# Optimization experiments

Measured on AMD Instinct MI355X. Metric: run time of the kernel, lower is better.

Reference implementation:

```python
import jax, jax.numpy as jnp
import numpy as np

INTERVAL = 4
Q = 2 ** INTERVAL          # 16, quantization step
L = 2 ** (8 - INTERVAL) + 1  # 17, LUT size per axis


def round_ste(x):
    # round in forward, identity in backward (BPDA)
    return x + jax.lax.stop_gradient(jnp.round(x) - x)


def setup_inputs() -> dict:
    key = jax.random.key(0)
    k1, k2, k3 = jax.random.split(key, 3)
    # pixel values in [0, 255)
    img = jax.random.uniform(k1, (2, 3, 1080, 1920), jnp.float32) * 255.0
    # int8 LUT / 127 -> values in [-1, 1], shape [L^3, 3, 1, 1]
    lut = jax.random.uniform(k2, (L ** 3, 3, 1, 1), jnp.float32, -1.0, 1.0)
    # color correction matrix, scaled so final output mostly lands in [0,1]
    ccm = (jnp.eye(3, dtype=jnp.float32) + 0.05 * jax.random.normal(k3, (3, 3), jnp.float32)) / 127.0
    return {"img": img, "lut": lut, "ccm": ccm}


def _lut3d_interp(img, lut):
    """Trilinear 3D-LUT interpolation (InterpTorch3DBatch). img: [B,3,H,W]."""
    B, C, H, W = img.shape
    # _prepare_3d_lut_weights: scale, round with STE, clamp
    w = jnp.clip(round_ste(lut * 127.0), -127.0, 127.0)[:, :, 0, 0]  # [L^3, 3]
    flat = img.transpose(0, 2, 3, 1).reshape(-1, 3)  # [N, 3] per-pixel rgb
    r, g, b = flat[:, 0], flat[:, 1], flat[:, 2]
    r1 = jnp.floor(r / Q).astype(jnp.int32)
    g1 = jnp.floor(g / Q).astype(jnp.int32)
    b1 = jnp.floor(b / Q).astype(jnp.int32)
    fr = jnp.mod(r, float(Q))
    fg = jnp.mod(g, float(Q))
    fb = jnp.mod(b, float(Q))
    r2 = jnp.clip(r1 + 1, 0, L - 1)
    g2 = jnp.clip(g1 + 1, 0, L - 1)
    b2 = jnp.clip(b1 + 1, 0, L - 1)

    def corner(i, j, k):
        return w[i * (L * L) + j * L + k]  # [N, 3] gather

    p000 = corner(r1, g1, b1); p001 = corner(r1, g1, b2)
    p010 = corner(r1, g2, b1); p011 = corner(r1, g2, b2)
    p100 = corner(r2, g1, b1); p101 = corner(r2, g1, b2)
    p110 = corner(r2, g2, b1); p111 = corner(r2, g2, b2)

    fr = (fr / Q)[:, None]; fg = (fg / Q)[:, None]; fb = (fb / Q)[:, None]
    c00 = p000 * (1 - fr) + p100 * fr
    c01 = p001 * (1 - fr) + p101 * fr
    c10 = p010 * (1 - fr) + p110 * fr
    c11 = p011 * (1 - fr) + p111 * fr
    c0 = c00 * (1 - fg) + c10 * fg
    c1 = c01 * (1 - fg) + c11 * fg
    out = c0 * (1 - fb) + c1 * fb  # [N, 3]
    return out, (B, H, W, C)


def reference(img, lut, ccm):
    out_pix, (B, H, W, C) = _lut3d_interp(img, lut)
    # apply_color: per-pixel 3x3 color matrix (tensordot dims [[-1],[-1]]) + clamp
    out_pix = jnp.clip(out_pix @ ccm.T, 1e-8, 1.0)
    return out_pix.reshape(B, H, W, C).transpose(0, 3, 1, 2)
```

## Files before the change

### kernel.cpp

```cpp
#include <hip/hip_runtime.h>
#include <cstdint>

#define LUT_L    17
#define LUT_LL   289
#define NLUT     4913
#define NLUT_PAD 4916
#define IMG_B    2
#define IMG_H    1080
#define IMG_W    1920
#define PLANE    (IMG_H * IMG_W)
#define NPIX     (IMG_B * PLANE)
#define NQUAD    (NPIX / 4)
#define QPB      512
#define NBLK     (NQUAD / QPB)

typedef float nfloat4 __attribute__((ext_vector_type(4)));

__device__ __forceinline__ int pack_entry_biased(const float* __restrict__ lut, int idx) {
    float r = lut[idx * 3 + 0] * 127.0f;
    float g = lut[idx * 3 + 1] * 127.0f;
    float b = lut[idx * 3 + 2] * 127.0f;
    int ir = (int)rintf(r);
    int ig = (int)rintf(g);
    int ib = (int)rintf(b);
    ir = max(-127, min(127, ir)) + 127;
    ig = max(-127, min(127, ig)) + 127;
    ib = max(-127, min(127, ib)) + 127;
    return ir | (ig << 8) | (ib << 16);
}

__global__ void pack_lut_kernel(const float* __restrict__ lut, int* __restrict__ wq) {
    int idx = blockIdx.x * blockDim.x + threadIdx.x;
    if (idx >= NLUT_PAD) return;
    wq[idx] = (idx < NLUT) ? pack_entry_biased(lut, idx) : 0;
}

__device__ __forceinline__ float ub0(int v) { return (float)( (unsigned)v        & 0xffu); }
__device__ __forceinline__ float ub1(int v) { return (float)(((unsigned)v >>  8) & 0xffu); }
__device__ __forceinline__ float ub2(int v) { return (float)(((unsigned)v >> 16) & 0xffu); }

__device__ __forceinline__ float clamp01eps(float x) {
    return fminf(fmaxf(x, 1e-8f), 1.0f);
}

__device__ __forceinline__ void px_process(float r, float g, float b,
                                           const int* wq,
                                           const float* __restrict__ m,
                                           const float* __restrict__ off,
                                           float& o0, float& o1, float& o2) {
    float rq = r * 0.0625f, gq = g * 0.0625f, bq = b * 0.0625f;
    float rf = floorf(rq), gf = floorf(gq), bf = floorf(bq);
    float fr = rq - rf, fg = gq - gf, fb = bq - bf;
    int i1 = (int)rf, j1 = (int)gf, k1 = (int)bf;

    const int* r00 = wq + (i1 * LUT_LL + j1 * LUT_L + k1);
    const int* r01 = r00 + LUT_L;
    const int* r10 = r00 + LUT_LL;
    const int* r11 = r10 + LUT_L;
    int w000 = r00[0], w001 = r00[1];
    int w010 = r01[0], w011 = r01[1];
    int w100 = r10[0], w101 = r10[1];
    int w110 = r11[0], w111 = r11[1];

    float wr0 = 1.0f - fr, wg0 = 1.0f - fg, wb0 = 1.0f - fb;
    float a00 = wg0 * wb0, a01 = wg0 * fb, a10 = fg * wb0, a11 = fg * fb;
    float s000 = wr0 * a00, s001 = wr0 * a01, s010 = wr0 * a10, s011 = wr0 * a11;
    float s100 = fr  * a00, s101 = fr  * a01, s110 = fr  * a10, s111 = fr  * a11;

    float pr = s000 * ub0(w000);
    pr = fmaf(s001, ub0(w001), pr); pr = fmaf(s010, ub0(w010), pr);
    pr = fmaf(s011, ub0(w011), pr); pr = fmaf(s100, ub0(w100), pr);
    pr = fmaf(s101, ub0(w101), pr); pr = fmaf(s110, ub0(w110), pr);
    pr = fmaf(s111, ub0(w111), pr);

    float pg = s000 * ub1(w000);
    pg = fmaf(s001, ub1(w001), pg); pg = fmaf(s010, ub1(w010), pg);
    pg = fmaf(s011, ub1(w011), pg); pg = fmaf(s100, ub1(w100), pg);
    pg = fmaf(s101, ub1(w101), pg); pg = fmaf(s110, ub1(w110), pg);
    pg = fmaf(s111, ub1(w111), pg);

    float pb = s000 * ub2(w000);
    pb = fmaf(s001, ub2(w001), pb); pb = fmaf(s010, ub2(w010), pb);
    pb = fmaf(s011, ub2(w011), pb); pb = fmaf(s100, ub2(w100), pb);
    pb = fmaf(s101, ub2(w101), pb); pb = fmaf(s110, ub2(w110), pb);
    pb = fmaf(s111, ub2(w111), pb);

    o0 = clamp01eps(fmaf(pr, m[0], fmaf(pg, m[1], fmaf(pb, m[2], off[0]))));
    o1 = clamp01eps(fmaf(pr, m[3], fmaf(pg, m[4], fmaf(pb, m[5], off[1]))));
    o2 = clamp01eps(fmaf(pr, m[6], fmaf(pg, m[7], fmaf(pb, m[8], off[2]))));
}

__device__ __forceinline__ void quad_addr(int q, size_t& base) {
    int p = q * 4;
    int bimg = p / PLANE;
    int hw = p - bimg * PLANE;
    base = (size_t)bimg * 3 * PLANE + hw;
}

__device__ __forceinline__ void quad_compute_store(float* __restrict__ out,
                                                   const int* wq,
                                                   const float* __restrict__ m,
                                                   const float* __restrict__ off,
                                                   size_t base,
                                                   nfloat4 R, nfloat4 G, nfloat4 Bv) {
    float o0x, o0y, o0z, o0w;
    float o1x, o1y, o1z, o1w;
    float o2x, o2y, o2z, o2w;

    px_process(R.x, G.x, Bv.x, wq, m, off, o0x, o1x, o2x);
    px_process(R.y, G.y, Bv.y, wq, m, off, o0y, o1y, o2y);
    px_process(R.z, G.z, Bv.z, wq, m, off, o0z, o1z, o2z);
    px_process(R.w, G.w, Bv.w, wq, m, off, o0w, o1w, o2w);

    nfloat4 O0 = {o0x, o0y, o0z, o0w};
    nfloat4 O1 = {o1x, o1y, o1z, o1w};
    nfloat4 O2 = {o2x, o2y, o2z, o2w};

    __builtin_nontemporal_store(O0, (nfloat4*)(out + base));
    __builtin_nontemporal_store(O1, (nfloat4*)(out + base + PLANE));
    __builtin_nontemporal_store(O2, (nfloat4*)(out + base + 2 * PLANE));
}

__global__ __launch_bounds__(256) void lut3d(const float* __restrict__ img,
                                             const int* __restrict__ wq_g,
                                             const float* __restrict__ ccm,
                                             float* __restrict__ out) {
    __shared__ int wq[NLUT_PAD];

    int q0 = blockIdx.x * QPB + threadIdx.x;
    int q1 = q0 + 256;
    size_t base0, base1;
    quad_addr(q0, base0);
    quad_addr(q1, base1);

    nfloat4 R0  = *(const nfloat4*)(img + base0);
    nfloat4 G0  = *(const nfloat4*)(img + base0 + PLANE);
    nfloat4 B0  = *(const nfloat4*)(img + base0 + 2 * PLANE);

    {
        const int4* src = (const int4*)wq_g;
        int4* dst = (int4*)wq;
        for (int i = threadIdx.x; i < NLUT_PAD / 4; i += 256) dst[i] = src[i];
    }
    float m[9], off[3];
#pragma unroll
    for (int i = 0; i < 9; i++) m[i] = ccm[i];
#pragma unroll
    for (int c = 0; c < 3; c++) off[c] = -127.0f * (m[3*c] + m[3*c+1] + m[3*c+2]);
    __syncthreads();

    quad_compute_store(out, wq, m, off, base0, R0, G0, B0);

    nfloat4 R1  = *(const nfloat4*)(img + base1);
    nfloat4 G1  = *(const nfloat4*)(img + base1 + PLANE);
    nfloat4 B1  = *(const nfloat4*)(img + base1 + 2 * PLANE);
    quad_compute_store(out, wq, m, off, base1, R1, G1, B1);
}

__global__ __launch_bounds__(256) void lut3d_build(const float* __restrict__ img,
                                                   const float* __restrict__ lut,
                                                   const float* __restrict__ ccm,
                                                   float* __restrict__ out) {
    __shared__ int wq[NLUT_PAD];
    for (int i = threadIdx.x; i < NLUT_PAD; i += 256)
        wq[i] = (i < NLUT) ? pack_entry_biased(lut, i) : 0;
    float m[9], off[3];
#pragma unroll
    for (int i = 0; i < 9; i++) m[i] = ccm[i];
#pragma unroll
    for (int c = 0; c < 3; c++) off[c] = -127.0f * (m[3*c] + m[3*c+1] + m[3*c+2]);
    __syncthreads();

    int q0 = blockIdx.x * QPB + threadIdx.x;
    int q1 = q0 + 256;
    size_t base0, base1;
    quad_addr(q0, base0);
    quad_addr(q1, base1);
    nfloat4 R0  = *(const nfloat4*)(img + base0);
    nfloat4 G0  = *(const nfloat4*)(img + base0 + PLANE);
    nfloat4 B0  = *(const nfloat4*)(img + base0 + 2 * PLANE);
    quad_compute_store(out, wq, m, off, base0, R0, G0, B0);
    nfloat4 R1  = *(const nfloat4*)(img + base1);
    nfloat4 G1  = *(const nfloat4*)(img + base1 + PLANE);
    nfloat4 B1  = *(const nfloat4*)(img + base1 + 2 * PLANE);
    quad_compute_store(out, wq, m, off, base1, R1, G1, B1);
}

extern "C" void kernel_launch(void* const* d_in, const int* in_sizes, int n_in,
                              void* d_out, int out_size, void* d_ws, size_t ws_size,
                              hipStream_t stream) {
    const float* img = (const float*)d_in[0];
    const float* lut = (const float*)d_in[1];
    const float* ccm = (const float*)d_in[2];
    float* out = (float*)d_out;

    if (ws_size >= NLUT_PAD * sizeof(int)) {
        int* wq = (int*)d_ws;
        pack_lut_kernel<<<(NLUT_PAD + 255) / 256, 256, 0, stream>>>(lut, wq);
        lut3d<<<NBLK, 256, 0, stream>>>(img, wq, ccm, out);
    } else {
        lut3d_build<<<NBLK, 256, 0, stream>>>(img, lut, ccm, out);
    }
}
```

Baseline: 106.5 us.

## Fuse LUT packing into main kernel and process four quads per thread

Removes the separate LUT pack kernel and its launch, so every block quantizes and packs the LUT from the float input straight into shared memory. Each block now covers 1024 quads instead of 512, which halves the number of blocks and the redundant per-block LUT build work. A tail block handles only the first two quads. The trade-off is that each block now does more scalar float loads and conversions for the LUT build, and the grid has less parallelism.

```diff
diff --git a/kernel.cpp b/kernel.cpp
--- a/kernel.cpp
+++ b/kernel.cpp
@@ -11,8 +11,8 @@
 #define PLANE    (IMG_H * IMG_W)
 #define NPIX     (IMG_B * PLANE)
 #define NQUAD    (NPIX / 4)
-#define QPB      512
-#define NBLK     (NQUAD / QPB)
+#define QPB      1024
+#define NFULL    (NQUAD / QPB)
 
 typedef float nfloat4 __attribute__((ext_vector_type(4)));
 
@@ -27,12 +27,6 @@
     ig = max(-127, min(127, ig)) + 127;
     ib = max(-127, min(127, ib)) + 127;
     return ir | (ig << 8) | (ib << 16);
-}
-
-__global__ void pack_lut_kernel(const float* __restrict__ lut, int* __restrict__ wq) {
-    int idx = blockIdx.x * blockDim.x + threadIdx.x;
-    if (idx >= NLUT_PAD) return;
-    wq[idx] = (idx < NLUT) ? pack_entry_biased(lut, idx) : 0;
 }
 
 __device__ __forceinline__ float ub0(int v) { return (float)( (unsigned)v        & 0xffu); }
@@ -90,11 +84,11 @@
     o2 = clamp01eps(fmaf(pr, m[6], fmaf(pg, m[7], fmaf(pb, m[8], off[2]))));
 }
 
-__device__ __forceinline__ void quad_addr(int q, size_t& base) {
+__device__ __forceinline__ size_t quad_addr(int q) {
     int p = q * 4;
     int bimg = p / PLANE;
     int hw = p - bimg * PLANE;
-    base = (size_t)bimg * 3 * PLANE + hw;
+    return (size_t)bimg * 3 * PLANE + hw;
 }
 
 __device__ __forceinline__ void quad_compute_store(float* __restrict__ out,
@@ -121,27 +115,35 @@
     __builtin_nontemporal_store(O2, (nfloat4*)(out + base + 2 * PLANE));
 }
 
-__global__ __launch_bounds__(256) void lut3d(const float* __restrict__ img,
-                                             const int* __restrict__ wq_g,
-                                             const float* __restrict__ ccm,
-                                             float* __restrict__ out) {
+__device__ __forceinline__ void do_quad(const float* __restrict__ img,
+                                        float* __restrict__ out,
+                                        const int* wq,
+                                        const float* __restrict__ m,
+                                        const float* __restrict__ off,
+                                        int q) {
+    size_t base = quad_addr(q);
+    nfloat4 R  = *(const nfloat4*)(img + base);
+    nfloat4 G  = *(const nfloat4*)(img + base + PLANE);
+    nfloat4 Bv = *(const nfloat4*)(img + base + 2 * PLANE);
+    quad_compute_store(out, wq, m, off, base, R, G, Bv);
+}
+
+__global__ __launch_bounds__(256) void lut3d_fused(const float* __restrict__ img,
+                                                   const float* __restrict__ lut,
+                                                   const float* __restrict__ ccm,
+                                                   float* __restrict__ out) {
     __shared__ int wq[NLUT_PAD];
 
     int q0 = blockIdx.x * QPB + threadIdx.x;
-    int q1 = q0 + 256;
-    size_t base0, base1;
-    quad_addr(q0, base0);
-    quad_addr(q1, base1);
+    size_t base0 = quad_addr(q0);
 
-    nfloat4 R0  = *(const nfloat4*)(img + base0);
-    nfloat4 G0  = *(const nfloat4*)(img + base0 + PLANE);
-    nfloat4 B0  = *(const nfloat4*)(img + base0 + 2 * PLANE);
+    nfloat4 R0 = *(const nfloat4*)(img + base0);
+    nfloat4 G0 = *(const nfloat4*)(img + base0 + PLANE);
+    nfloat4 B0 = *(const nfloat4*)(img + base0 + 2 * PLANE);
 
-    {
-        const int4* src = (const int4*)wq_g;
-        int4* dst = (int4*)wq;
-        for (int i = threadIdx.x; i < NLUT_PAD / 4; i += 256) dst[i] = src[i];
-    }
+    for (int i = threadIdx.x; i < NLUT; i += 256)
+        wq[i] = pack_entry_biased(lut, i);
+
     float m[9], off[3];
 #pragma unroll
     for (int i = 0; i < 9; i++) m[i] = ccm[i];
@@ -150,40 +152,12 @@
     __syncthreads();
 
     quad_compute_store(out, wq, m, off, base0, R0, G0, B0);
+    do_quad(img, out, wq, m, off, q0 + 256);
 
-    nfloat4 R1  = *(const nfloat4*)(img + base1);
-    nfloat4 G1  = *(const nfloat4*)(img + base1 + PLANE);
-    nfloat4 B1  = *(const nfloat4*)(img + base1 + 2 * PLANE);
-    quad_compute_store(out, wq, m, off, base1, R1, G1, B1);
-}
-
-__global__ __launch_bounds__(256) void lut3d_build(const float* __restrict__ img,
-                                                   const float* __restrict__ lut,
-                                                   const float* __restrict__ ccm,
-                                                   float* __restrict__ out) {
-    __shared__ int wq[NLUT_PAD];
-    for (int i = threadIdx.x; i < NLUT_PAD; i += 256)
-        wq[i] = (i < NLUT) ? pack_entry_biased(lut, i) : 0;
-    float m[9], off[3];
-#pragma unroll
-    for (int i = 0; i < 9; i++) m[i] = ccm[i];
-#pragma unroll
-    for (int c = 0; c < 3; c++) off[c] = -127.0f * (m[3*c] + m[3*c+1] + m[3*c+2]);
-    __syncthreads();
-
-    int q0 = blockIdx.x * QPB + threadIdx.x;
-    int q1 = q0 + 256;
-    size_t base0, base1;
-    quad_addr(q0, base0);
-    quad_addr(q1, base1);
-    nfloat4 R0  = *(const nfloat4*)(img + base0);
-    nfloat4 G0  = *(const nfloat4*)(img + base0 + PLANE);
-    nfloat4 B0  = *(const nfloat4*)(img + base0 + 2 * PLANE);
-    quad_compute_store(out, wq, m, off, base0, R0, G0, B0);
-    nfloat4 R1  = *(const nfloat4*)(img + base1);
-    nfloat4 G1  = *(const nfloat4*)(img + base1 + PLANE);
-    nfloat4 B1  = *(const nfloat4*)(img + base1 + 2 * PLANE);
-    quad_compute_store(out, wq, m, off, base1, R1, G1, B1);
+    if (blockIdx.x < NFULL) {
+        do_quad(img, out, wq, m, off, q0 + 512);
+        do_quad(img, out, wq, m, off, q0 + 768);
+    }
 }
 
 extern "C" void kernel_launch(void* const* d_in, const int* in_sizes, int n_in,
@@ -194,11 +168,6 @@
     const float* ccm = (const float*)d_in[2];
     float* out = (float*)d_out;
 
-    if (ws_size >= NLUT_PAD * sizeof(int)) {
-        int* wq = (int*)d_ws;
-        pack_lut_kernel<<<(NLUT_PAD + 255) / 256, 256, 0, stream>>>(lut, wq);
-        lut3d<<<NBLK, 256, 0, stream>>>(img, wq, ccm, out);
-    } else {
-        lut3d_build<<<NBLK, 256, 0, stream>>>(img, lut, ccm, out);
-    }
+    const int grid = NFULL + 1;
+    lut3d_fused<<<grid, 256, 0, stream>>>(img, lut, ccm, out);
 }
```

After: 108.9 us. 1.02x slower.
